# Optimization experiments

Hardware: AMD Instinct MI355X
Metric: run time of the kernel (lower is better)

The kernel has to match this reference:

```python
import jax, jax.numpy as jnp
import numpy as np

B = 8192          # sessions
DOCS = 10         # docs per session
NPS = 21          # nodes per session: 1 query + 10 docs + 10 titles
N = B * NPS       # 172032 total nodes
F_IN, F_HID, F_OUT = 171, 256, 128


def _gat_conv(x, src, dst, W, a_src, a_dst, bias, n_nodes):
    # PyG GATConv, heads=1, negative_slope=0.2, self-loops already appended.
    h = x @ W.T                                   # [N, F]
    e = jax.nn.leaky_relu(jnp.take(h @ a_src, src) + jnp.take(h @ a_dst, dst), 0.2)
    m = jax.ops.segment_max(e, dst, num_segments=n_nodes)
    ex = jnp.exp(e - m[dst])
    denom = jax.ops.segment_sum(ex, dst, num_segments=n_nodes)
    alpha = ex / denom[dst]                       # softmax over incoming edges
    out = jax.ops.segment_sum(h[src] * alpha[:, None], dst, num_segments=n_nodes)
    return out + bias


def setup_inputs() -> dict:
    key = jax.random.key(0)
    ks = jax.random.split(key, 20)
    # structured node ids: per session block [q, d0..d9, t0..t9]
    base = jnp.arange(B, dtype=jnp.int64) * NPS
    doc_id = base[:, None] + 1 + jnp.arange(DOCS, dtype=jnp.int64)   # [B,10]
    q = base                                                          # query node = doc_id[:,0]-1
    t = doc_id + DOCS                                                 # title node = doc+10
    qd_s = jnp.repeat(q, DOCS); qd_d = doc_id.reshape(-1)
    dt_s = doc_id.reshape(-1);  dt_d = t.reshape(-1)
    src = jnp.concatenate([qd_s, qd_d, dt_s, dt_d])
    dst = jnp.concatenate([qd_d, qd_s, dt_d, dt_s])
    edge_index = jnp.stack([src, dst])                                # [2, 327680]

    inp = {
        "i": 0,
        "x": jax.random.normal(ks[0], (N, F_IN), jnp.float32),
        "edge_index": edge_index,
        "doc_id": doc_id,
        "click": jax.random.randint(ks[1], (B,), 0, 2),
        "query": jax.random.randint(ks[2], (B,), 0, 6338),
        "docu": jax.random.randint(ks[3], (B, DOCS), 0, 56477),
        "title_id": jax.random.randint(ks[4], (B, DOCS), 0, 56363),
        # embedding tables
        "query_table": jax.random.normal(ks[5], (6338, 160), jnp.float32) * 0.02,
        "doc_table": jax.random.normal(ks[6], (56477, 160), jnp.float32) * 0.02,
        "title_table": jax.random.normal(ks[7], (56363, 160), jnp.float32) * 0.02,
        "pos_table": jax.random.normal(ks[8], (10, 1), jnp.float32) * 0.02,
        "click_table": jax.random.normal(ks[9], (2, 1), jnp.float32) * 0.02,
        # GATConv 1 (171 -> 256)
        "W1": jax.random.normal(ks[10], (F_HID, F_IN), jnp.float32) * (1.0 / np.sqrt(F_IN)),
        "a_src1": jax.random.normal(ks[11], (F_HID,), jnp.float32) * 0.1,
        "a_dst1": jax.random.normal(ks[12], (F_HID,), jnp.float32) * 0.1,
        "b1": jnp.zeros((F_HID,), jnp.float32),
        # GATConv 2 (256 -> 128)
        "W2": jax.random.normal(ks[13], (F_OUT, F_HID), jnp.float32) * (1.0 / np.sqrt(F_HID)),
        "a_src2": jax.random.normal(ks[14], (F_OUT,), jnp.float32) * 0.1,
        "a_dst2": jax.random.normal(ks[15], (F_OUT,), jnp.float32) * 0.1,
        "b2": jnp.zeros((F_OUT,), jnp.float32),
        # head linear (128 -> 1)
        "Wl": jax.random.normal(ks[16], (1, F_OUT), jnp.float32) * (1.0 / np.sqrt(F_OUT)),
        "bl": jnp.zeros((1,), jnp.float32),
    }
    return inp


def reference(i, x, edge_index, doc_id, click, query, docu, title_id,
              query_table, doc_table, title_table, pos_table, click_table,
              W1, a_src1, a_dst1, b1, W2, a_src2, a_dst2, b2, Wl, bl):
    n_nodes = x.shape[0]
    q_emb = query_table[query]          # [B,160]
    d_emb = doc_table[docu]             # [B,10,160]
    t_emb = title_table[title_id]       # [B,10,160]
    pos = pos_table[:, 0]               # [10]  (position_embedding of 0..9)
    clk = click_table[click, 0]         # [B]

    df = doc_id.reshape(-1)             # flat doc node ids [B*10]
    if i == 0:
        x = x.at[doc_id[:, 0] - 1, :160].set(q_emb)
        x = x.at[df, :160].set(d_emb.reshape(-1, 160))
        x = x.at[df, 160].set(jnp.broadcast_to(pos, doc_id.shape).reshape(-1))
        x = x.at[df, 161 + i].set(jnp.broadcast_to(clk[:, None], doc_id.shape).reshape(-1))
        x = x.at[df + 10, :160].set(t_emb.reshape(-1, 160))
    else:
        x = x.at[df, 161 + i].set(jnp.broadcast_to(clk[:, None], doc_id.shape).reshape(-1))

    # add self-loops (PyG GATConv default)
    loop = jnp.arange(n_nodes, dtype=edge_index.dtype)
    src = jnp.concatenate([edge_index[0], loop])
    dst = jnp.concatenate([edge_index[1], loop])

    y = _gat_conv(x, src, dst, W1, a_src1, a_dst1, b1, n_nodes)
    y = jax.nn.relu(y)                  # dropout is identity in eval mode
    hidden_state = _gat_conv(y, src, dst, W2, a_src2, a_dst2, b2, n_nodes)
    y = jax.nn.relu(hidden_state)
    y = jax.nn.sigmoid(y @ Wl.T + bl)   # [N,1]
    return (hidden_state, y, x[:, :171])
```

## Files before the change

kernel.cpp:

```cpp
#include <hip/hip_runtime.h>
#include <cstdint>

#define N_NODES 172032
#define BATCH   8192
#define NPS     21
#define F_IN    171
#define K1P     192
#define F_HID   256
#define F_OUT   128
#define SX_F    (NPS * F_IN)
#define SXB     (NPS * K1P)

typedef unsigned short u16;
typedef __attribute__((ext_vector_type(8))) short  bf16x8;
typedef __attribute__((ext_vector_type(4))) float  f32x4;

__device__ inline u16 f2bf(float f) {
    unsigned u = __float_as_uint(f);
    unsigned r = u + 0x7FFFu + ((u >> 16) & 1u);
    return (u16)(r >> 16);
}
__device__ inline float bf2f(u16 h) { return __uint_as_float(((unsigned)h) << 16); }
__device__ inline float lrelu(float v) { return v > 0.f ? v : 0.2f * v; }

__device__ inline int deg_of(int n)  { return n == 0 ? 11 : (n <= 10 ? 3 : 2); }
__device__ inline int edge_base(int n) { return n == 0 ? 0 : (n <= 10 ? 11 + 3*(n-1) : 41 + 2*(n-11)); }
__device__ inline int src_of(int n, int k) {
    if (n == 0)  return k < 10 ? k + 1 : 0;
    if (n <= 10) return k == 0 ? 0 : (k == 1 ? n + 10 : n);
    return k == 0 ? n - 10 : n;
}

__device__ inline float wave_red(float v) {
    for (int off = 32; off; off >>= 1) v += __shfl_down(v, off);
    return v;
}

__global__ __launch_bounds__(256) void build_x(const int* __restrict__ iptr, const float* __restrict__ x,
                        const int* __restrict__ click, const int* __restrict__ query,
                        const int* __restrict__ docu, const int* __restrict__ title_id,
                        const float* __restrict__ qtab, const float* __restrict__ dtab,
                        const float* __restrict__ ttab, const float* __restrict__ ptab,
                        const float* __restrict__ ctab,
                        float* __restrict__ out_x, u16* __restrict__ xb)
{
    __shared__ float sx[SX_F];
    __shared__ int   dz[10], tz[10], s_q;
    __shared__ float s_clk;

    const int s   = blockIdx.x;
    const int tid = threadIdx.x;
    const int i   = iptr[0];
    const long xbase = (long)s * SX_F;

    if (tid < 10)       dz[tid]      = docu[s*10 + tid];
    else if (tid < 20)  tz[tid - 10] = title_id[s*10 + tid - 10];
    else if (tid == 20) s_q          = query[s];
    else if (tid == 21) s_clk        = ctab[click[s]];
    __syncthreads();

    if (i == 0) {
        for (int idx = tid; idx < SX_F; idx += 256) {
            int p = idx / F_IN;
            int c = idx - p * F_IN;
            float v;
            if (c >= 160) {
                if (p >= 1 && p <= 10 && c == 160)      v = ptab[p - 1];
                else if (p >= 1 && p <= 10 && c == 161) v = s_clk;
                else                                     v = x[xbase + idx];
            } else {
                if (p == 0)       v = qtab[(long)s_q * 160 + c];
                else if (p <= 10) v = dtab[(long)dz[p-1] * 160 + c];
                else              v = ttab[(long)tz[p-11] * 160 + c];
            }
            sx[idx] = v;
        }
    } else {
        for (int idx = tid; idx < SX_F; idx += 256) {
            int p = idx / F_IN;
            int c = idx - p * F_IN;
            float v = x[xbase + idx];
            if (p >= 1 && p <= 10 && c == 161 + i) v = s_clk;
            sx[idx] = v;
        }
    }
    __syncthreads();

    {
        int r    = (int)(xbase & 3);
        int head = (4 - r) & 3;
        if (tid < head) out_x[xbase + tid] = sx[tid];
        int n4 = (SX_F - head) >> 2;
        for (int id = tid; id < n4; id += 256) {
            int o = head + id * 4;
            float4 v = make_float4(sx[o], sx[o+1], sx[o+2], sx[o+3]);
            *(float4*)(out_x + xbase + o) = v;
        }
        int done = head + n4 * 4;
        int tail = SX_F - done;
        if (tid < tail) out_x[xbase + done + tid] = sx[done + tid];
    }

    {
        u16* xbs = xb + (long)s * SXB;
        for (int id = tid; id < SXB / 8; id += 256) {
            int k0 = id * 8;
            int node = k0 / K1P;
            int kk   = k0 - node * K1P;
            union { u16 h[8]; uint4 v; } u;
            #pragma unroll
            for (int j = 0; j < 8; ++j) {
                int c = kk + j;
                u.h[j] = (c < F_IN) ? f2bf(sx[node * F_IN + c]) : (u16)0;
            }
            *(uint4*)(xbs + k0) = u.v;
        }
    }
}

__global__ void prep_w(const float* __restrict__ W1, const float* __restrict__ W2,
                       u16* __restrict__ W1b, u16* __restrict__ W2b)
{
    int id = blockIdx.x * 256 + threadIdx.x;
    if (id < 256 * K1P) {
        int r = id / K1P, k = id - r * K1P;
        W1b[id] = (k < F_IN) ? f2bf(W1[r * F_IN + k]) : (u16)0;
    }
    if (id < 128 * 256) W2b[id] = f2bf(W2[id]);
}

template<int KPAD, int KSTAGE>
__global__ __launch_bounds__(256) void gemm_bt(const u16* __restrict__ A, const u16* __restrict__ B,
                                               u16* __restrict__ C, int ldc)
{
    constexpr int SA  = KSTAGE + 8;
    constexpr int CPS = KSTAGE / 8;
    __shared__ __align__(16) u16 Al[64 * SA];
    __shared__ __align__(16) u16 Bl[128 * SA];

    const int m0 = blockIdx.x * 64;
    const int n0 = blockIdx.y * 128;
    const int tid = threadIdx.x;
    const int lane = tid & 63, w = tid >> 6;
    const int wr = w >> 1, wc = w & 1;
    const int lm = lane & 15, lq = lane >> 4;

    f32x4 acc[2][4];
    for (int f = 0; f < 2; ++f)
        for (int g = 0; g < 4; ++g)
            acc[f][g] = (f32x4){0.f, 0.f, 0.f, 0.f};

    for (int ks = 0; ks < KPAD; ks += KSTAGE) {
        if (ks) __syncthreads();
        for (int id = tid; id < 64 * CPS; id += 256) {
            int row = id / CPS, ch = id - row * CPS;
            uint4 vv = *(const uint4*)(A + (long)(m0 + row) * KPAD + ks + ch * 8);
            *(uint4*)(Al + row * SA + ch * 8) = vv;
        }
        for (int id = tid; id < 128 * CPS; id += 256) {
            int row = id / CPS, ch = id - row * CPS;
            uint4 vv = *(const uint4*)(B + (long)(n0 + row) * KPAD + ks + ch * 8);
            *(uint4*)(Bl + row * SA + ch * 8) = vv;
        }
        __syncthreads();

        for (int kb = 0; kb < KSTAGE / 32; ++kb) {
            int koff = kb * 32 + lq * 8;
            bf16x8 a0 = *(const bf16x8*)(Al + (wr*32 +  0 + lm) * SA + koff);
            bf16x8 a1 = *(const bf16x8*)(Al + (wr*32 + 16 + lm) * SA + koff);
            bf16x8 b0 = *(const bf16x8*)(Bl + (wc*64 +  0 + lm) * SA + koff);
            bf16x8 b1 = *(const bf16x8*)(Bl + (wc*64 + 16 + lm) * SA + koff);
            bf16x8 b2 = *(const bf16x8*)(Bl + (wc*64 + 32 + lm) * SA + koff);
            bf16x8 b3 = *(const bf16x8*)(Bl + (wc*64 + 48 + lm) * SA + koff);
            acc[0][0] = __builtin_amdgcn_mfma_f32_16x16x32_bf16(a0, b0, acc[0][0], 0, 0, 0);
            acc[0][1] = __builtin_amdgcn_mfma_f32_16x16x32_bf16(a0, b1, acc[0][1], 0, 0, 0);
            acc[0][2] = __builtin_amdgcn_mfma_f32_16x16x32_bf16(a0, b2, acc[0][2], 0, 0, 0);
            acc[0][3] = __builtin_amdgcn_mfma_f32_16x16x32_bf16(a0, b3, acc[0][3], 0, 0, 0);
            acc[1][0] = __builtin_amdgcn_mfma_f32_16x16x32_bf16(a1, b0, acc[1][0], 0, 0, 0);
            acc[1][1] = __builtin_amdgcn_mfma_f32_16x16x32_bf16(a1, b1, acc[1][1], 0, 0, 0);
            acc[1][2] = __builtin_amdgcn_mfma_f32_16x16x32_bf16(a1, b2, acc[1][2], 0, 0, 0);
            acc[1][3] = __builtin_amdgcn_mfma_f32_16x16x32_bf16(a1, b3, acc[1][3], 0, 0, 0);
        }
    }

    for (int f = 0; f < 2; ++f)
        for (int g = 0; g < 4; ++g)
            for (int r = 0; r < 4; ++r) {
                int row = m0 + wr*32 + f*16 + lq*4 + r;
                int col = n0 + wc*64 + g*16 + lm;
                C[(long)row * ldc + col] = f2bf(acc[f][g][r]);
            }
}

__global__ __launch_bounds__(256) void agg1(const u16* __restrict__ h1b,
                                            const float* __restrict__ asrc, const float* __restrict__ adst,
                                            const float* __restrict__ bias, u16* __restrict__ y1b)
{
    __shared__ __align__(16) u16 h[NPS * F_HID];
    __shared__ float s_l[NPS], d_l[NPS], alpha[61];
    int blk = blockIdx.x, tid = threadIdx.x;
    long base = (long)blk * NPS * F_HID;

    for (int id = tid; id < NPS * F_HID / 8; id += 256)
        *(uint4*)(h + id * 8) = *(const uint4*)(h1b + base + id * 8);
    __syncthreads();

    int lane = tid & 63, w = tid >> 6;
    for (int n = w; n < NPS; n += 4) {
        float as_ = 0.f, ad_ = 0.f;
        for (int c = lane; c < F_HID; c += 64) {
            float hv = bf2f(h[n * F_HID + c]);
            as_ += hv * asrc[c];
            ad_ += hv * adst[c];
        }
        as_ = wave_red(as_); ad_ = wave_red(ad_);
        if (lane == 0) { s_l[n] = as_; d_l[n] = ad_; }
    }
    __syncthreads();

    if (tid < NPS) {
        int n = tid, deg = deg_of(n), eb = edge_base(n);
        float dn = d_l[n], m = -1e30f;
        for (int k = 0; k < deg; ++k) m = fmaxf(m, lrelu(s_l[src_of(n,k)] + dn));
        float den = 0.f;
        for (int k = 0; k < deg; ++k) den += expf(lrelu(s_l[src_of(n,k)] + dn) - m);
        float inv = 1.f / den;
        for (int k = 0; k < deg; ++k) alpha[eb + k] = expf(lrelu(s_l[src_of(n,k)] + dn) - m) * inv;
    }
    __syncthreads();

    int c = tid;
    {
        float a = alpha[10] * bf2f(h[c]);
        for (int j = 1; j <= 10; ++j) a += alpha[j-1] * bf2f(h[j * F_HID + c]);
        y1b[base + c] = f2bf(fmaxf(a + bias[c], 0.f));
    }
    for (int j = 1; j <= 10; ++j) {
        int eb = 11 + 3*(j-1);
        float a = alpha[eb]   * bf2f(h[c])
                + alpha[eb+1] * bf2f(h[(j+10) * F_HID + c])
                + alpha[eb+2] * bf2f(h[j * F_HID + c]);
        y1b[base + j * F_HID + c] = f2bf(fmaxf(a + bias[c], 0.f));
    }
    for (int j = 1; j <= 10; ++j) {
        int eb = 41 + 2*(j-1);
        float a = alpha[eb]   * bf2f(h[j * F_HID + c])
                + alpha[eb+1] * bf2f(h[(10+j) * F_HID + c]);
        y1b[base + (10+j) * F_HID + c] = f2bf(fmaxf(a + bias[c], 0.f));
    }
}

__global__ __launch_bounds__(128) void agg2(const u16* __restrict__ g2b,
                                            const float* __restrict__ asrc, const float* __restrict__ adst,
                                            const float* __restrict__ bias,
                                            const float* __restrict__ Wl, const float* __restrict__ bl,
                                            float* __restrict__ out_hid, float* __restrict__ out_y)
{
    __shared__ __align__(16) u16 h[NPS * F_OUT];
    __shared__ float s_l[NPS], d_l[NPS], alpha[61];
    __shared__ float hid[NPS * F_OUT];
    int blk = blockIdx.x, tid = threadIdx.x;
    long base = (long)blk * NPS * F_OUT;

    for (int id = tid; id < NPS * F_OUT / 8; id += 128)
        *(uint4*)(h + id * 8) = *(const uint4*)(g2b + base + id * 8);
    __syncthreads();

    int lane = tid & 63, w = tid >> 6;
    for (int n = w; n < NPS; n += 2) {
        float as_ = 0.f, ad_ = 0.f;
        for (int c = lane; c < F_OUT; c += 64) {
            float hv = bf2f(h[n * F_OUT + c]);
            as_ += hv * asrc[c];
            ad_ += hv * adst[c];
        }
        as_ = wave_red(as_); ad_ = wave_red(ad_);
        if (lane == 0) { s_l[n] = as_; d_l[n] = ad_; }
    }
    __syncthreads();

    if (tid < NPS) {
        int n = tid, deg = deg_of(n), eb = edge_base(n);
        float dn = d_l[n], m = -1e30f;
        for (int k = 0; k < deg; ++k) m = fmaxf(m, lrelu(s_l[src_of(n,k)] + dn));
        float den = 0.f;
        for (int k = 0; k < deg; ++k) den += expf(lrelu(s_l[src_of(n,k)] + dn) - m);
        float inv = 1.f / den;
        for (int k = 0; k < deg; ++k) alpha[eb + k] = expf(lrelu(s_l[src_of(n,k)] + dn) - m) * inv;
    }
    __syncthreads();

    int c = tid;
    float wl = Wl[c];
    {
        float a = alpha[10] * bf2f(h[c]);
        for (int j = 1; j <= 10; ++j) a += alpha[j-1] * bf2f(h[j * F_OUT + c]);
        float hv = a + bias[c];
        out_hid[base + c] = hv;
        hid[c] = fmaxf(hv, 0.f) * wl;
    }
    for (int j = 1; j <= 10; ++j) {
        int eb = 11 + 3*(j-1);
        float a = alpha[eb]   * bf2f(h[c])
                + alpha[eb+1] * bf2f(h[(j+10) * F_OUT + c])
                + alpha[eb+2] * bf2f(h[j * F_OUT + c]);
        float hv = a + bias[c];
        out_hid[base + j * F_OUT + c] = hv;
        hid[j * F_OUT + c] = fmaxf(hv, 0.f) * wl;
    }
    for (int j = 1; j <= 10; ++j) {
        int eb = 41 + 2*(j-1);
        float a = alpha[eb]   * bf2f(h[j * F_OUT + c])
                + alpha[eb+1] * bf2f(h[(10+j) * F_OUT + c]);
        float hv = a + bias[c];
        out_hid[base + (10+j) * F_OUT + c] = hv;
        hid[(10+j) * F_OUT + c] = fmaxf(hv, 0.f) * wl;
    }
    __syncthreads();

    float bl0 = bl[0];
    for (int n = w; n < NPS; n += 2) {
        float v = hid[n * F_OUT + lane] + hid[n * F_OUT + lane + 64];
        v = wave_red(v);
        if (lane == 0) out_y[(long)blk * NPS + n] = 1.f / (1.f + expf(-(v + bl0)));
    }
}

extern "C" void kernel_launch(void* const* d_in, const int* in_sizes, int n_in,
                              void* d_out, int out_size, void* d_ws, size_t ws_size,
                              hipStream_t stream) {
    const int*   ip    = (const int*)  d_in[0];
    const float* x     = (const float*)d_in[1];
    const int*   click = (const int*)  d_in[4];
    const int*   query = (const int*)  d_in[5];
    const int*   docu  = (const int*)  d_in[6];
    const int*   title = (const int*)  d_in[7];
    const float* qtab  = (const float*)d_in[8];
    const float* dtab  = (const float*)d_in[9];
    const float* ttab  = (const float*)d_in[10];
    const float* ptab  = (const float*)d_in[11];
    const float* ctab  = (const float*)d_in[12];
    const float* W1    = (const float*)d_in[13];
    const float* as1   = (const float*)d_in[14];
    const float* ad1   = (const float*)d_in[15];
    const float* b1    = (const float*)d_in[16];
    const float* W2    = (const float*)d_in[17];
    const float* as2   = (const float*)d_in[18];
    const float* ad2   = (const float*)d_in[19];
    const float* b2    = (const float*)d_in[20];
    const float* Wl    = (const float*)d_in[21];
    const float* bl    = (const float*)d_in[22];

    float* out_hid = (float*)d_out;
    float* out_y   = out_hid + (long)N_NODES * F_OUT;
    float* out_x   = out_y + N_NODES;

    u16* h1b = (u16*)d_ws;
    u16* g2b = h1b;
    u16* xb  = h1b + 44040192L;
    u16* y1b = xb;
    u16* W1b = h1b + 88080384L;
    u16* W2b = W1b + 256 * K1P;

    build_x<<<BATCH, 256, 0, stream>>>(ip, x, click, query, docu, title,
                                       qtab, dtab, ttab, ptab, ctab, out_x, xb);
    prep_w<<<192, 256, 0, stream>>>(W1, W2, W1b, W2b);
    gemm_bt<K1P, 96><<<dim3(N_NODES / 64, 2), 256, 0, stream>>>(xb, W1b, h1b, F_HID);
    agg1<<<BATCH, 256, 0, stream>>>(h1b, as1, ad1, b1, y1b);
    gemm_bt<F_HID, 128><<<dim3(N_NODES / 64, 1), 256, 0, stream>>>(y1b, W2b, g2b, F_OUT);
    agg2<<<BATCH, 128, 0, stream>>>(g2b, as2, ad2, b2, Wl, bl, out_hid, out_y);
}
```

Before: 588.2 us.

## Fuse GEMMs with GAT aggregation per 3-session block and merge weight prep

Each GEMM is fused with its attention aggregation into one kernel that handles three sessions (63 rows, padded to 64) per block. The h1 and g2 intermediates now stay in shared memory instead of going through global memory. The weight conversion is folded into build_x as extra blocks, so two kernel launches go away. The trade-off is a padded row per tile, larger shared-memory use per block that may lower occupancy, and W1 being reloaded from L2 by every block.

```diff
diff --git a/kernel.cpp b/kernel.cpp
--- a/kernel.cpp
+++ b/kernel.cpp
@@ -10,6 +10,8 @@
 #define F_OUT   128
 #define SX_F    (NPS * F_IN)
 #define SXB     (NPS * K1P)
+#define SPB     3
+#define NBLK    2731
 
 typedef unsigned short u16;
 typedef __attribute__((ext_vector_type(8))) short  bf16x8;
@@ -42,8 +44,20 @@
                         const float* __restrict__ qtab, const float* __restrict__ dtab,
                         const float* __restrict__ ttab, const float* __restrict__ ptab,
                         const float* __restrict__ ctab,
-                        float* __restrict__ out_x, u16* __restrict__ xb)
+                        const float* __restrict__ W1, const float* __restrict__ W2,
+                        float* __restrict__ out_x, u16* __restrict__ xb,
+                        u16* __restrict__ W1b, u16* __restrict__ W2b)
 {
+    if (blockIdx.x >= BATCH) {
+        int id = (blockIdx.x - BATCH) * 256 + threadIdx.x;
+        if (id < 256 * K1P) {
+            int r = id / K1P, k = id - r * K1P;
+            W1b[id] = (k < F_IN) ? f2bf(W1[r * F_IN + k]) : (u16)0;
+        }
+        if (id < 128 * 256) W2b[id] = f2bf(W2[id]);
+        return;
+    }
+
     __shared__ float sx[SX_F];
     __shared__ int   dz[10], tz[10], s_q;
     __shared__ float s_clk;
@@ -118,211 +132,265 @@
     }
 }
 
-__global__ void prep_w(const float* __restrict__ W1, const float* __restrict__ W2,
-                       u16* __restrict__ W1b, u16* __restrict__ W2b)
+__global__ __launch_bounds__(256) void fused1(const u16* __restrict__ xb, const u16* __restrict__ W1b,
+                                              const float* __restrict__ asrc, const float* __restrict__ adst,
+                                              const float* __restrict__ bias, u16* __restrict__ y1b)
 {
-    int id = blockIdx.x * 256 + threadIdx.x;
-    if (id < 256 * K1P) {
-        int r = id / K1P, k = id - r * K1P;
-        W1b[id] = (k < F_IN) ? f2bf(W1[r * F_IN + k]) : (u16)0;
-    }
-    if (id < 128 * 256) W2b[id] = f2bf(W2[id]);
-}
-
-template<int KPAD, int KSTAGE>
-__global__ __launch_bounds__(256) void gemm_bt(const u16* __restrict__ A, const u16* __restrict__ B,
-                                               u16* __restrict__ C, int ldc)
-{
-    constexpr int SA  = KSTAGE + 8;
-    constexpr int CPS = KSTAGE / 8;
+    constexpr int KS  = 64;
+    constexpr int SA  = 200;
+    constexpr int SB  = 72;
     __shared__ __align__(16) u16 Al[64 * SA];
-    __shared__ __align__(16) u16 Bl[128 * SA];
-
-    const int m0 = blockIdx.x * 64;
-    const int n0 = blockIdx.y * 128;
-    const int tid = threadIdx.x;
+    __shared__ __align__(16) u16 Bu[256 * SB];
+    __shared__ float s_l[64], d_l[64], alpha[3 * 61];
+
+    const int blk = blockIdx.x, tid = threadIdx.x;
+    const int s0  = blk * SPB;
+    const int nsamp = (s0 + SPB <= BATCH) ? SPB : (BATCH - s0);
+    const int nrow  = nsamp * NPS;
+
     const int lane = tid & 63, w = tid >> 6;
     const int wr = w >> 1, wc = w & 1;
     const int lm = lane & 15, lq = lane >> 4;
 
+    const u16* Ag = xb + (long)s0 * SXB;
+    for (int id = tid; id < 64 * (K1P / 8); id += 256) {
+        int row = id / 24, ch = id - row * 24;
+        uint4 v;
+        if (row < nrow) v = *(const uint4*)(Ag + row * K1P + ch * 8);
+        else            v = make_uint4(0u, 0u, 0u, 0u);
+        *(uint4*)(Al + row * SA + ch * 8) = v;
+    }
+
+    f32x4 acc[2][8];
+    #pragma unroll
+    for (int f = 0; f < 2; ++f)
+        #pragma unroll
+        for (int g = 0; g < 8; ++g)
+            acc[f][g] = (f32x4){0.f, 0.f, 0.f, 0.f};
+
+    for (int ks = 0; ks < K1P; ks += KS) {
+        __syncthreads();
+        for (int id = tid; id < 256 * (KS / 8); id += 256) {
+            int row = id >> 3, ch = id & 7;
+            *(uint4*)(Bu + row * SB + ch * 8) = *(const uint4*)(W1b + row * K1P + ks + ch * 8);
+        }
+        __syncthreads();
+        #pragma unroll
+        for (int kb = 0; kb < KS / 32; ++kb) {
+            int ka    = ks + kb * 32 + lq * 8;
+            int kboff = kb * 32 + lq * 8;
+            bf16x8 a0 = *(const bf16x8*)(Al + (wr*32 +  0 + lm) * SA + ka);
+            bf16x8 a1 = *(const bf16x8*)(Al + (wr*32 + 16 + lm) * SA + ka);
+            #pragma unroll
+            for (int g = 0; g < 8; ++g) {
+                bf16x8 b = *(const bf16x8*)(Bu + (wc*128 + g*16 + lm) * SB + kboff);
+                acc[0][g] = __builtin_amdgcn_mfma_f32_16x16x32_bf16(a0, b, acc[0][g], 0, 0, 0);
+                acc[1][g] = __builtin_amdgcn_mfma_f32_16x16x32_bf16(a1, b, acc[1][g], 0, 0, 0);
+            }
+        }
+    }
+
+    __syncthreads();
+    u16* h = Bu;
+    #pragma unroll
+    for (int f = 0; f < 2; ++f)
+        #pragma unroll
+        for (int g = 0; g < 8; ++g)
+            #pragma unroll
+            for (int r = 0; r < 4; ++r) {
+                int row = wr*32 + f*16 + lq*4 + r;
+                int col = wc*128 + g*16 + lm;
+                h[row * F_HID + col] = f2bf(acc[f][g][r]);
+            }
+    __syncthreads();
+
+    float av[4], dv[4];
+    #pragma unroll
+    for (int j = 0; j < 4; ++j) { av[j] = asrc[lane + j*64]; dv[j] = adst[lane + j*64]; }
+    for (int n = w; n < nrow; n += 4) {
+        float as_ = 0.f, ad_ = 0.f;
+        #pragma unroll
+        for (int j = 0; j < 4; ++j) {
+            float hv = bf2f(h[n * F_HID + lane + j*64]);
+            as_ += hv * av[j];
+            ad_ += hv * dv[j];
+        }
+        as_ = wave_red(as_); ad_ = wave_red(ad_);
+        if (lane == 0) { s_l[n] = as_; d_l[n] = ad_; }
+    }
+    __syncthreads();
+
+    if (tid < nrow) {
+        int s = tid / NPS, p = tid - s * NPS;
+        int deg = deg_of(p), eb = edge_base(p);
+        const float* sl = s_l + s * NPS;
+        float dn = d_l[tid], m = -1e30f;
+        for (int k = 0; k < deg; ++k) m = fmaxf(m, lrelu(sl[src_of(p,k)] + dn));
+        float den = 0.f;
+        for (int k = 0; k < deg; ++k) den += expf(lrelu(sl[src_of(p,k)] + dn) - m);
+        float inv = 1.f / den;
+        for (int k = 0; k < deg; ++k) alpha[s*61 + eb + k] = expf(lrelu(sl[src_of(p,k)] + dn) - m) * inv;
+    }
+    __syncthreads();
+
+    const int c = tid;
+    float bc = bias[c];
+    for (int s = 0; s < nsamp; ++s) {
+        const u16* hs = h + s * NPS * F_HID;
+        const float* al = alpha + s * 61;
+        u16* outp = y1b + ((long)(s0 + s) * NPS) * F_HID;
+        {
+            float a = al[10] * bf2f(hs[c]);
+            #pragma unroll
+            for (int j = 1; j <= 10; ++j) a += al[j-1] * bf2f(hs[j * F_HID + c]);
+            outp[c] = f2bf(fmaxf(a + bc, 0.f));
+        }
+        #pragma unroll
+        for (int j = 1; j <= 10; ++j) {
+            int eb = 11 + 3*(j-1);
+            float a = al[eb]   * bf2f(hs[c])
+                    + al[eb+1] * bf2f(hs[(j+10) * F_HID + c])
+                    + al[eb+2] * bf2f(hs[j * F_HID + c]);
+            outp[j * F_HID + c] = f2bf(fmaxf(a + bc, 0.f));
+        }
+        #pragma unroll
+        for (int j = 1; j <= 10; ++j) {
+            int eb = 41 + 2*(j-1);
+            float a = al[eb]   * bf2f(hs[j * F_HID + c])
+                    + al[eb+1] * bf2f(hs[(10+j) * F_HID + c]);
+            outp[(10+j) * F_HID + c] = f2bf(fmaxf(a + bc, 0.f));
+        }
+    }
+}
+
+__global__ __launch_bounds__(256) void fused2(const u16* __restrict__ y1b, const u16* __restrict__ W2b,
+                                              const float* __restrict__ asrc, const float* __restrict__ adst,
+                                              const float* __restrict__ bias,
+                                              const float* __restrict__ Wl, const float* __restrict__ bl,
+                                              float* __restrict__ out_hid, float* __restrict__ out_y)
+{
+    constexpr int KS  = 64;
+    constexpr int SA  = 264;
+    constexpr int SB  = 72;
+    __shared__ __align__(16) u16 Al[64 * SA];
+    __shared__ __align__(16) u16 Bu[128 * SB];
+    __shared__ float s_l[64], d_l[64], alpha[3 * 61];
+
+    const int blk = blockIdx.x, tid = threadIdx.x;
+    const int s0  = blk * SPB;
+    const int nsamp = (s0 + SPB <= BATCH) ? SPB : (BATCH - s0);
+    const int nrow  = nsamp * NPS;
+
+    const int lane = tid & 63, w = tid >> 6;
+    const int wr = w >> 1, wc = w & 1;
+    const int lm = lane & 15, lq = lane >> 4;
+
+    const u16* Ag = y1b + (long)s0 * NPS * F_HID;
+    for (int id = tid; id < 64 * (F_HID / 8); id += 256) {
+        int row = id >> 5, ch = id & 31;
+        uint4 v;
+        if (row < nrow) v = *(const uint4*)(Ag + row * F_HID + ch * 8);
+        else            v = make_uint4(0u, 0u, 0u, 0u);
+        *(uint4*)(Al + row * SA + ch * 8) = v;
+    }
+
     f32x4 acc[2][4];
+    #pragma unroll
     for (int f = 0; f < 2; ++f)
+        #pragma unroll
         for (int g = 0; g < 4; ++g)
             acc[f][g] = (f32x4){0.f, 0.f, 0.f, 0.f};
 
-    for (int ks = 0; ks < KPAD; ks += KSTAGE) {
-        if (ks) __syncthreads();
-        for (int id = tid; id < 64 * CPS; id += 256) {
-            int row = id / CPS, ch = id - row * CPS;
-            uint4 vv = *(const uint4*)(A + (long)(m0 + row) * KPAD + ks + ch * 8);
-            *(uint4*)(Al + row * SA + ch * 8) = vv;
-        }
-        for (int id = tid; id < 128 * CPS; id += 256) {
-            int row = id / CPS, ch = id - row * CPS;
-            uint4 vv = *(const uint4*)(B + (long)(n0 + row) * KPAD + ks + ch * 8);
-            *(uint4*)(Bl + row * SA + ch * 8) = vv;
-        }
+    for (int ks = 0; ks < F_HID; ks += KS) {
         __syncthreads();
-
-        for (int kb = 0; kb < KSTAGE / 32; ++kb) {
-            int koff = kb * 32 + lq * 8;
-            bf16x8 a0 = *(const bf16x8*)(Al + (wr*32 +  0 + lm) * SA + koff);
-            bf16x8 a1 = *(const bf16x8*)(Al + (wr*32 + 16 + lm) * SA + koff);
-            bf16x8 b0 = *(const bf16x8*)(Bl + (wc*64 +  0 + lm) * SA + koff);
-            bf16x8 b1 = *(const bf16x8*)(Bl + (wc*64 + 16 + lm) * SA + koff);
-            bf16x8 b2 = *(const bf16x8*)(Bl + (wc*64 + 32 + lm) * SA + koff);
-            bf16x8 b3 = *(const bf16x8*)(Bl + (wc*64 + 48 + lm) * SA + koff);
-            acc[0][0] = __builtin_amdgcn_mfma_f32_16x16x32_bf16(a0, b0, acc[0][0], 0, 0, 0);
-            acc[0][1] = __builtin_amdgcn_mfma_f32_16x16x32_bf16(a0, b1, acc[0][1], 0, 0, 0);
-            acc[0][2] = __builtin_amdgcn_mfma_f32_16x16x32_bf16(a0, b2, acc[0][2], 0, 0, 0);
-            acc[0][3] = __builtin_amdgcn_mfma_f32_16x16x32_bf16(a0, b3, acc[0][3], 0, 0, 0);
-            acc[1][0] = __builtin_amdgcn_mfma_f32_16x16x32_bf16(a1, b0, acc[1][0], 0, 0, 0);
-            acc[1][1] = __builtin_amdgcn_mfma_f32_16x16x32_bf16(a1, b1, acc[1][1], 0, 0, 0);
-            acc[1][2] = __builtin_amdgcn_mfma_f32_16x16x32_bf16(a1, b2, acc[1][2], 0, 0, 0);
-            acc[1][3] = __builtin_amdgcn_mfma_f32_16x16x32_bf16(a1, b3, acc[1][3], 0, 0, 0);
-        }
-    }
-
+        for (int id = tid; id < 128 * (KS / 8); id += 256) {
+            int row = id >> 3, ch = id & 7;
+            *(uint4*)(Bu + row * SB + ch * 8) = *(const uint4*)(W2b + row * F_HID + ks + ch * 8);
+        }
+        __syncthreads();
+        #pragma unroll
+        for (int kb = 0; kb < KS / 32; ++kb) {
+            int ka    = ks + kb * 32 + lq * 8;
+            int kboff = kb * 32 + lq * 8;
+            bf16x8 a0 = *(const bf16x8*)(Al + (wr*32 +  0 + lm) * SA + ka);
+            bf16x8 a1 = *(const bf16x8*)(Al + (wr*32 + 16 + lm) * SA + ka);
+            #pragma unroll
+            for (int g = 0; g < 4; ++g) {
+                bf16x8 b = *(const bf16x8*)(Bu + (wc*64 + g*16 + lm) * SB + kboff);
+                acc[0][g] = __builtin_amdgcn_mfma_f32_16x16x32_bf16(a0, b, acc[0][g], 0, 0, 0);
+                acc[1][g] = __builtin_amdgcn_mfma_f32_16x16x32_bf16(a1, b, acc[1][g], 0, 0, 0);
+            }
+        }
+    }
+
+    __syncthreads();
+    u16* h2 = Bu;
+    #pragma unroll
     for (int f = 0; f < 2; ++f)
+        #pragma unroll
         for (int g = 0; g < 4; ++g)
+            #pragma unroll
             for (int r = 0; r < 4; ++r) {
-                int row = m0 + wr*32 + f*16 + lq*4 + r;
-                int col = n0 + wc*64 + g*16 + lm;
-                C[(long)row * ldc + col] = f2bf(acc[f][g][r]);
-            }
-}
-
-__global__ __launch_bounds__(256) void agg1(const u16* __restrict__ h1b,
-                                            const float* __restrict__ asrc, const float* __restrict__ adst,
-                                            const float* __restrict__ bias, u16* __restrict__ y1b)
-{
-    __shared__ __align__(16) u16 h[NPS * F_HID];
-    __shared__ float s_l[NPS], d_l[NPS], alpha[61];
-    int blk = blockIdx.x, tid = threadIdx.x;
-    long base = (long)blk * NPS * F_HID;
-
-    for (int id = tid; id < NPS * F_HID / 8; id += 256)
-        *(uint4*)(h + id * 8) = *(const uint4*)(h1b + base + id * 8);
-    __syncthreads();
-
-    int lane = tid & 63, w = tid >> 6;
-    for (int n = w; n < NPS; n += 4) {
+                int row = wr*32 + f*16 + lq*4 + r;
+                int col = wc*64 + g*16 + lm;
+                h2[row * F_OUT + col] = f2bf(acc[f][g][r]);
+            }
+    __syncthreads();
+
+    float av[2], dv[2];
+    #pragma unroll
+    for (int j = 0; j < 2; ++j) { av[j] = asrc[lane + j*64]; dv[j] = adst[lane + j*64]; }
+    for (int n = w; n < nrow; n += 4) {
         float as_ = 0.f, ad_ = 0.f;
-        for (int c = lane; c < F_HID; c += 64) {
-            float hv = bf2f(h[n * F_HID + c]);
-            as_ += hv * asrc[c];
-            ad_ += hv * adst[c];
+        #pragma unroll
+        for (int j = 0; j < 2; ++j) {
+            float hv = bf2f(h2[n * F_OUT + lane + j*64]);
+            as_ += hv * av[j];
+            ad_ += hv * dv[j];
         }
         as_ = wave_red(as_); ad_ = wave_red(ad_);
         if (lane == 0) { s_l[n] = as_; d_l[n] = ad_; }
     }
     __syncthreads();
 
-    if (tid < NPS) {
-        int n = tid, deg = deg_of(n), eb = edge_base(n);
-        float dn = d_l[n], m = -1e30f;
-        for (int k = 0; k < deg; ++k) m = fmaxf(m, lrelu(s_l[src_of(n,k)] + dn));
+    if (tid < nrow) {
+        int s = tid / NPS, p = tid - s * NPS;
+        int deg = deg_of(p), eb = edge_base(p);
+        const float* sl = s_l + s * NPS;
+        float dn = d_l[tid], m = -1e30f;
+        for (int k = 0; k < deg; ++k) m = fmaxf(m, lrelu(sl[src_of(p,k)] + dn));
         float den = 0.f;
-        for (int k = 0; k < deg; ++k) den += expf(lrelu(s_l[src_of(n,k)] + dn) - m);
+        for (int k = 0; k < deg; ++k) den += expf(lrelu(sl[src_of(p,k)] + dn) - m);
         float inv = 1.f / den;
-        for (int k = 0; k < deg; ++k) alpha[eb + k] = expf(lrelu(s_l[src_of(n,k)] + dn) - m) * inv;
-    }
-    __syncthreads();
-
-    int c = tid;
-    {
-        float a = alpha[10] * bf2f(h[c]);
-        for (int j = 1; j <= 10; ++j) a += alpha[j-1] * bf2f(h[j * F_HID + c]);
-        y1b[base + c] = f2bf(fmaxf(a + bias[c], 0.f));
-    }
-    for (int j = 1; j <= 10; ++j) {
-        int eb = 11 + 3*(j-1);
-        float a = alpha[eb]   * bf2f(h[c])
-                + alpha[eb+1] * bf2f(h[(j+10) * F_HID + c])
-                + alpha[eb+2] * bf2f(h[j * F_HID + c]);
-        y1b[base + j * F_HID + c] = f2bf(fmaxf(a + bias[c], 0.f));
-    }
-    for (int j = 1; j <= 10; ++j) {
-        int eb = 41 + 2*(j-1);
-        float a = alpha[eb]   * bf2f(h[j * F_HID + c])
-                + alpha[eb+1] * bf2f(h[(10+j) * F_HID + c]);
-        y1b[base + (10+j) * F_HID + c] = f2bf(fmaxf(a + bias[c], 0.f));
-    }
-}
-
-__global__ __launch_bounds__(128) void agg2(const u16* __restrict__ g2b,
-                                            const float* __restrict__ asrc, const float* __restrict__ adst,
-                                            const float* __restrict__ bias,
-                                            const float* __restrict__ Wl, const float* __restrict__ bl,
-                                            float* __restrict__ out_hid, float* __restrict__ out_y)
-{
-    __shared__ __align__(16) u16 h[NPS * F_OUT];
-    __shared__ float s_l[NPS], d_l[NPS], alpha[61];
-    __shared__ float hid[NPS * F_OUT];
-    int blk = blockIdx.x, tid = threadIdx.x;
-    long base = (long)blk * NPS * F_OUT;
-
-    for (int id = tid; id < NPS * F_OUT / 8; id += 128)
-        *(uint4*)(h + id * 8) = *(const uint4*)(g2b + base + id * 8);
-    __syncthreads();
-
-    int lane = tid & 63, w = tid >> 6;
-    for (int n = w; n < NPS; n += 2) {
-        float as_ = 0.f, ad_ = 0.f;
-        for (int c = lane; c < F_OUT; c += 64) {
-            float hv = bf2f(h[n * F_OUT + c]);
-            as_ += hv * asrc[c];
-            ad_ += hv * adst[c];
-        }
-        as_ = wave_red(as_); ad_ = wave_red(ad_);
-        if (lane == 0) { s_l[n] = as_; d_l[n] = ad_; }
-    }
-    __syncthreads();
-
-    if (tid < NPS) {
-        int n = tid, deg = deg_of(n), eb = edge_base(n);
-        float dn = d_l[n], m = -1e30f;
-        for (int k = 0; k < deg; ++k) m = fmaxf(m, lrelu(s_l[src_of(n,k)] + dn));
-        float den = 0.f;
-        for (int k = 0; k < deg; ++k) den += expf(lrelu(s_l[src_of(n,k)] + dn) - m);
-        float inv = 1.f / den;
-        for (int k = 0; k < deg; ++k) alpha[eb + k] = expf(lrelu(s_l[src_of(n,k)] + dn) - m) * inv;
-    }
-    __syncthreads();
-
-    int c = tid;
+        for (int k = 0; k < deg; ++k) alpha[s*61 + eb + k] = expf(lrelu(sl[src_of(p,k)] + dn) - m) * inv;
+    }
+    __syncthreads();
+
+    float* hidwl = (float*)Al;
+    const int c    = tid & 127;
+    const int half = tid >> 7;
+    float bc = bias[c];
     float wl = Wl[c];
-    {
-        float a = alpha[10] * bf2f(h[c]);
-        for (int j = 1; j <= 10; ++j) a += alpha[j-1] * bf2f(h[j * F_OUT + c]);
-        float hv = a + bias[c];
-        out_hid[base + c] = hv;
-        hid[c] = fmaxf(hv, 0.f) * wl;
-    }
-    for (int j = 1; j <= 10; ++j) {
-        int eb = 11 + 3*(j-1);
-        float a = alpha[eb]   * bf2f(h[c])
-                + alpha[eb+1] * bf2f(h[(j+10) * F_OUT + c])
-                + alpha[eb+2] * bf2f(h[j * F_OUT + c]);
-        float hv = a + bias[c];
-        out_hid[base + j * F_OUT + c] = hv;
-        hid[j * F_OUT + c] = fmaxf(hv, 0.f) * wl;
-    }
-    for (int j = 1; j <= 10; ++j) {
-        int eb = 41 + 2*(j-1);
-        float a = alpha[eb]   * bf2f(h[j * F_OUT + c])
-                + alpha[eb+1] * bf2f(h[(10+j) * F_OUT + c]);
-        float hv = a + bias[c];
-        out_hid[base + (10+j) * F_OUT + c] = hv;
-        hid[(10+j) * F_OUT + c] = fmaxf(hv, 0.f) * wl;
+    for (int s = 0; s < nsamp; ++s) {
+        const u16* hs = h2 + s * NPS * F_OUT;
+        const float* al = alpha + s * 61;
+        long gb = (long)(s0 + s) * NPS * F_OUT;
+        for (int p = half; p < NPS; p += 2) {
+            int deg = deg_of(p), eb = edge_base(p);
+            float a = 0.f;
+            for (int k = 0; k < deg; ++k) a += al[eb + k] * bf2f(hs[src_of(p,k) * F_OUT + c]);
+            float hv = a + bc;
+            out_hid[gb + p * F_OUT + c] = hv;
+            hidwl[(s * NPS + p) * F_OUT + c] = fmaxf(hv, 0.f) * wl;
+        }
     }
     __syncthreads();
 
     float bl0 = bl[0];
-    for (int n = w; n < NPS; n += 2) {
-        float v = hid[n * F_OUT + lane] + hid[n * F_OUT + lane + 64];
+    for (int n = w; n < nrow; n += 4) {
+        float v = hidwl[n * F_OUT + lane] + hidwl[n * F_OUT + lane + 64];
         v = wave_red(v);
-        if (lane == 0) out_y[(long)blk * NPS + n] = 1.f / (1.f + expf(-(v + bl0)));
+        if (lane == 0) out_y[(long)s0 * NPS + n] = 1.f / (1.f + expf(-(v + bl0)));
     }
 }
 
@@ -355,18 +423,14 @@
     float* out_y   = out_hid + (long)N_NODES * F_OUT;
     float* out_x   = out_y + N_NODES;
 
-    u16* h1b = (u16*)d_ws;
-    u16* g2b = h1b;
-    u16* xb  = h1b + 44040192L;
-    u16* y1b = xb;
-    u16* W1b = h1b + 88080384L;
+    u16* xb  = (u16*)d_ws;
+    u16* y1b = xb + (long)BATCH * SXB;
+    u16* W1b = y1b + (long)N_NODES * F_HID;
     u16* W2b = W1b + 256 * K1P;
 
-    build_x<<<BATCH, 256, 0, stream>>>(ip, x, click, query, docu, title,
-                                       qtab, dtab, ttab, ptab, ctab, out_x, xb);
-    prep_w<<<192, 256, 0, stream>>>(W1, W2, W1b, W2b);
-    gemm_bt<K1P, 96><<<dim3(N_NODES / 64, 2), 256, 0, stream>>>(xb, W1b, h1b, F_HID);
-    agg1<<<BATCH, 256, 0, stream>>>(h1b, as1, ad1, b1, y1b);
-    gemm_bt<F_HID, 128><<<dim3(N_NODES / 64, 1), 256, 0, stream>>>(y1b, W2b, g2b, F_OUT);
-    agg2<<<BATCH, 128, 0, stream>>>(g2b, as2, ad2, b2, Wl, bl, out_hid, out_y);
-}
+    build_x<<<BATCH + 192, 256, 0, stream>>>(ip, x, click, query, docu, title,
+                                             qtab, dtab, ttab, ptab, ctab,
+                                             W1, W2, out_x, xb, W1b, W2b);
+    fused1<<<NBLK, 256, 0, stream>>>(xb, W1b, as1, ad1, b1, y1b);
+    fused2<<<NBLK, 256, 0, stream>>>(y1b, W2b, as2, ad2, b2, Wl, bl, out_hid, out_y);
+}
```

Result: slower. 645.5 us (+9.7%).
